# Kernel optimization log

Hardware: AMD Instinct MI355X
Metric: run time of the kernel (lower is better)

Reference implementation:

```python
import jax, jax.numpy as jnp
import numpy as np

PH = PW = 5  # roi_size
EPS = 1e-5


def _conv1x1(x, w, b):
    # x: (B,Cin,H,W), w: (Cout,Cin)
    return jnp.einsum('bchw,oc->bohw', x, w) + b[None, :, None, None]


def _resize_ac(x, oh, ow):
    # F.interpolate bilinear, align_corners=True. x: (B,C,H,W)
    B, C, H, W = x.shape
    ys = jnp.linspace(0.0, H - 1.0, oh)
    xs = jnp.linspace(0.0, W - 1.0, ow)
    y0 = jnp.floor(ys).astype(jnp.int32); y1 = jnp.minimum(y0 + 1, H - 1)
    x0 = jnp.floor(xs).astype(jnp.int32); x1 = jnp.minimum(x0 + 1, W - 1)
    ly = (ys - y0)[:, None]; lx = (xs - x0)[None, :]
    v00 = x[:, :, y0[:, None], x0[None, :]]
    v01 = x[:, :, y0[:, None], x1[None, :]]
    v10 = x[:, :, y1[:, None], x0[None, :]]
    v11 = x[:, :, y1[:, None], x1[None, :]]
    return v00 * (1 - ly) * (1 - lx) + v01 * (1 - ly) * lx + v10 * ly * (1 - lx) + v11 * ly * lx


def _roi_align_one(feat, box):
    # torchvision RoIAlign, spatial_scale=1, sampling_ratio=1, aligned=False
    # feat: (C,H,W), box: (x1,y1,x2,y2)
    C, H, W = feat.shape
    bx1, by1, bx2, by2 = box[0], box[1], box[2], box[3]
    rw = jnp.maximum(bx2 - bx1, 1.0)
    rh = jnp.maximum(by2 - by1, 1.0)
    xs = bx1 + (jnp.arange(PW, dtype=feat.dtype) + 0.5) * (rw / PW)
    ys = by1 + (jnp.arange(PH, dtype=feat.dtype) + 0.5) * (rh / PH)
    yg = jnp.broadcast_to(ys[:, None], (PH, PW))
    xg = jnp.broadcast_to(xs[None, :], (PH, PW))
    valid = (yg >= -1.0) & (yg <= H) & (xg >= -1.0) & (xg <= W)
    y = jnp.clip(yg, 0.0, H - 1.0); x = jnp.clip(xg, 0.0, W - 1.0)
    y0 = jnp.floor(y).astype(jnp.int32); x0 = jnp.floor(x).astype(jnp.int32)
    y1i = jnp.minimum(y0 + 1, H - 1); x1i = jnp.minimum(x0 + 1, W - 1)
    ly = y - y0; lx = x - x0
    v = (feat[:, y0, x0] * (1 - ly) * (1 - lx) + feat[:, y0, x1i] * (1 - ly) * lx
         + feat[:, y1i, x0] * ly * (1 - lx) + feat[:, y1i, x1i] * ly * lx)
    return v * valid  # (C,PH,PW)


def _layernorm(x, w, b):
    mu = jnp.mean(x, -1, keepdims=True)
    var = jnp.var(x, -1, keepdims=True)
    return (x - mu) * jax.lax.rsqrt(var + EPS) * w + b


def setup_inputs() -> dict:
    key = jax.random.key(0)
    ks = jax.random.split(key, 16)
    B, G, NB, HF = 8, 8, 16, 28
    x4 = jax.random.normal(ks[0], (B, 1024, 14, 14), jnp.float32)
    x5 = jax.random.normal(ks[1], (B, 2048, 7, 7), jnp.float32)
    bx = jax.random.uniform(ks[2], (B, NB), minval=0.0, maxval=18.0)
    by = jax.random.uniform(ks[3], (B, NB), minval=0.0, maxval=18.0)
    bw = jax.random.uniform(ks[4], (B, NB), minval=3.0, maxval=10.0)
    bh = jax.random.uniform(ks[5], (B, NB), minval=3.0, maxval=10.0)
    boxes = jnp.stack([bx, by, jnp.minimum(bx + bw, 28.0), jnp.minimum(by + bh, 28.0)], -1)
    group = jax.random.randint(ks[6], (B, G, 2), 0, NB, jnp.int32)
    real_in_num = jnp.full((B,), G, jnp.int32)
    label_s = jax.random.randint(ks[7], (B, G), 0, 6, jnp.int64)
    label_s = jnp.where(jnp.arange(G)[None, :] % 3 == 0, -1, label_s)  # exercise both branches
    skeleton = jax.random.normal(ks[8], (B, G, HF, HF), jnp.float32)
    D = 1536 * PH * PW  # 38400
    return {
        'x4': x4, 'x5': x5, 'boxes': boxes, 'skeleton': skeleton,
        'group': group, 'real_in_num': real_in_num, 'label_s': label_s,
        'conv1_w': jax.random.normal(ks[9], (), jnp.float32) * 0.5,
        'conv1_b': jax.random.normal(ks[10], (), jnp.float32) * 0.1,
        'conv2_w': jax.random.normal(ks[11], (512, 1024), jnp.float32) * 0.03,
        'conv2_b': jnp.zeros((512,), jnp.float32),
        'conv3_w': jax.random.normal(ks[12], (1024, 2048), jnp.float32) * 0.02,
        'conv3_b': jnp.zeros((1024,), jnp.float32),
        'norm1_w': jnp.ones((D,), jnp.float32), 'norm1_b': jnp.zeros((D,), jnp.float32),
        'norm2_w': jnp.ones((512,), jnp.float32), 'norm2_b': jnp.zeros((512,), jnp.float32),
        'fc1_w': jax.random.normal(ks[13], (512, D), jnp.float32) * float(np.sqrt(2.0 / D)),
        'fc1_b': jnp.zeros((512,), jnp.float32),
        'fc2_w': jax.random.normal(ks[14], (6, 512), jnp.float32) * float(np.sqrt(2.0 / 512)),
        'fc2_b': jnp.zeros((6,), jnp.float32),
    }


def reference(x4, x5, boxes, skeleton, group, real_in_num, label_s,
              conv1_w, conv1_b, conv2_w, conv2_b, conv3_w, conv3_b,
              norm1_w, norm1_b, norm2_w, norm2_b, fc1_w, fc1_b, fc2_w, fc2_b):
    B, G = skeleton.shape[0], skeleton.shape[1]
    HF, WF = skeleton.shape[2], skeleton.shape[3]
    # backbone heads: 1x1 conv + bilinear upsample (align_corners=True), concat
    f4 = _resize_ac(_conv1x1(x4, conv2_w, conv2_b), HF, WF)   # (B,512,28,28)
    f5 = _resize_ac(_conv1x1(x5, conv3_w, conv3_b), HF, WF)   # (B,1024,28,28)
    app = jnp.concatenate([f4, f5], axis=1)                   # (B,1536,28,28)
    C = app.shape[1]
    # per-person pose gate: 1x1 conv (scalar on single channel) + sigmoid
    gate = jax.nn.sigmoid(skeleton * conv1_w + conv1_b)       # (B,G,28,28)
    gated = gate[:, :, None] * app[:, None]                   # (B,G,C,28,28)
    use_gate = (label_s != -1)[:, :, None, None, None]
    pose_feature = jnp.where(use_gate, gated, app[:, None])   # (B,G,C,28,28)
    # union box of the two interacting people (get_box_tensor)
    bidx = jnp.arange(B)[:, None]
    b1 = boxes[bidx, group[..., 0]]                           # (B,G,4)
    b2 = boxes[bidx, group[..., 1]]
    ub = jnp.stack([jnp.minimum(b1[..., 0], b2[..., 0]), jnp.minimum(b1[..., 1], b2[..., 1]),
                    jnp.maximum(b1[..., 2], b2[..., 2]), jnp.maximum(b1[..., 3], b2[..., 3])], -1)
    # batched RoIAlign over all N = B*G boxes
    feats = pose_feature.reshape(B * G, C, HF, WF)
    rois = jax.vmap(_roi_align_one)(feats, ub.reshape(B * G, 4))  # (N,C,5,5)
    sk = rois.reshape(B * G, -1)                              # (N,38400)
    sk = jax.nn.relu(_layernorm(sk, norm1_w, norm1_b))
    # dropout(p=0.9) is identity in eval mode
    sk = sk @ fc1_w.T + fc1_b
    sk = _layernorm(sk, norm2_w, norm2_b)
    score = sk @ fc2_w.T + fc2_b                              # (N,6)
    return score
```

## Files before the change

kernel.cpp:

```cpp
#include <hip/hip_runtime.h>
#include <math.h>

#define B8   8
#define HW4  196
#define HW5  49
#define HFW  28
#define NPIX 784
#define CAPP 1536
#define D1   38400
#define NR   64

typedef short short8 __attribute__((ext_vector_type(8)));
typedef short short4v __attribute__((ext_vector_type(4)));
typedef float floatx16 __attribute__((ext_vector_type(16)));

__device__ __forceinline__ unsigned short f2bf(float f) {
  unsigned u = __float_as_uint(f);
  u += 0x7FFF + ((u >> 16) & 1);
  return (unsigned short)(u >> 16);
}

struct Params {
  const float *x4, *x5, *boxes, *skel;
  const int *group, *label;
  const float *c1w, *c1b, *w2c, *b2c, *w3c, *b3c;
  const float *n1w, *n1b, *n2w, *n2b, *fw1, *fb1, *fw2, *fb2;
  float* out;
  unsigned short *x4T, *x5T, *sknT;
  float *f4T, *f5T, *tap4w, *tap5w, *descw, *roisP, *stats, *out1;
  int *tap4o, *tap5o, *desco;
};

union SharedU {
  float tile[32 * 201];
  struct {
    unsigned short As[2][4096];
    unsigned short Bs[2][4096];
  } g;
  struct {
    float cw4[16], cw5[16], wgs;
    int co4[16], co5[16];
    float red[8];
  } roi;
  struct {
    float red[8];
    float red2[24];
  } ln;
};

__device__ __forceinline__ void gemm_unit(
    SharedU& sh, const unsigned short* __restrict__ A, const float* __restrict__ Bw,
    float* __restrict__ C, int mt, int nt, int k0, int kchunk,
    int K, int N, int Mvalid) {
  int t = threadIdx.x;
  int wave = t >> 6, lane = t & 63;
  int wm = wave & 1, wn = wave >> 1;
  const unsigned short* Aptr = A + (size_t)(mt * 64) * K + k0;
  const float* Bptr = Bw + (size_t)(nt * 64) * K + k0;
  short8 areg[2];
  float4 breg[4];
  floatx16 acc;
#pragma unroll
  for (int i = 0; i < 16; i++) acc[i] = 0.f;
  int nkb = kchunk >> 6;

#pragma unroll
  for (int i = 0; i < 2; i++) {
    int e = t + i * 256;
    areg[i] = *(const short8*)(Aptr + (size_t)(e >> 3) * K + (e & 7) * 8);
  }
#pragma unroll
  for (int i = 0; i < 4; i++) {
    int e = t + i * 256;
    breg[i] = *(const float4*)(Bptr + (size_t)(e >> 4) * K + (e & 15) * 4);
  }
#pragma unroll
  for (int i = 0; i < 2; i++) {
    int e = t + i * 256;
    int m = e >> 3, ko = e & 7;
    *(short8*)&sh.g.As[0][ko * 512 + ((m ^ ko)) * 8] = areg[i];
  }
#pragma unroll
  for (int i = 0; i < 4; i++) {
    int e = t + i * 256;
    short4v v;
    v[0] = (short)f2bf(breg[i].x); v[1] = (short)f2bf(breg[i].y);
    v[2] = (short)f2bf(breg[i].z); v[3] = (short)f2bf(breg[i].w);
    int ko = (e & 15) >> 1, half = (e & 15) & 1, n = e >> 4;
    *(short4v*)&sh.g.Bs[0][ko * 512 + ((n ^ ko)) * 8 + half * 4] = v;
  }
  __syncthreads();

  for (int kb = 0; kb < nkb; kb++) {
    int buf = kb & 1;
    bool more = (kb + 1) < nkb;
    if (more) {
      int kof = (kb + 1) * 64;
#pragma unroll
      for (int i = 0; i < 2; i++) {
        int e = t + i * 256;
        areg[i] = *(const short8*)(Aptr + (size_t)(e >> 3) * K + kof + (e & 7) * 8);
      }
#pragma unroll
      for (int i = 0; i < 4; i++) {
        int e = t + i * 256;
        breg[i] = *(const float4*)(Bptr + (size_t)(e >> 4) * K + kof + (e & 15) * 4);
      }
    }
#pragma unroll
    for (int s = 0; s < 4; s++) {
      int ko = 2 * s + (lane >> 5);
      int am = wm * 32 + (lane & 31);
      int bn = wn * 32 + (lane & 31);
      short8 af = *(const short8*)&sh.g.As[buf][ko * 512 + ((am ^ ko)) * 8];
      short8 bf = *(const short8*)&sh.g.Bs[buf][ko * 512 + ((bn ^ ko)) * 8];
      acc = __builtin_amdgcn_mfma_f32_32x32x16_bf16(af, bf, acc, 0, 0, 0);
    }
    __syncthreads();
    if (more) {
      int nb2 = 1 - buf;
#pragma unroll
      for (int i = 0; i < 2; i++) {
        int e = t + i * 256;
        int m = e >> 3, ko = e & 7;
        *(short8*)&sh.g.As[nb2][ko * 512 + ((m ^ ko)) * 8] = areg[i];
      }
#pragma unroll
      for (int i = 0; i < 4; i++) {
        int e = t + i * 256;
        short4v v;
        v[0] = (short)f2bf(breg[i].x); v[1] = (short)f2bf(breg[i].y);
        v[2] = (short)f2bf(breg[i].z); v[3] = (short)f2bf(breg[i].w);
        int ko = (e & 15) >> 1, half = (e & 15) & 1, n = e >> 4;
        *(short4v*)&sh.g.Bs[nb2][ko * 512 + ((n ^ ko)) * 8 + half * 4] = v;
      }
      __syncthreads();
    }
  }

  int col = nt * 64 + wn * 32 + (lane & 31);
  int rbase = mt * 64 + wm * 32 + 4 * (lane >> 5);
#pragma unroll
  for (int reg = 0; reg < 16; reg++) {
    int row = rbase + (reg & 3) + 8 * (reg >> 2);
    if (row < Mvalid) atomicAdd(&C[(size_t)row * N + col], acc[reg]);
  }
}

__device__ __forceinline__ float gate_val(const float* sk, int yy, int xx,
                                          float c1w, float c1b, bool use) {
  if (!use) return 1.f;
  float z = sk[yy * HFW + xx] * c1w + c1b;
  return 1.f / (1.f + expf(-z));
}

__device__ void run_phase(const Params& p, int phase, SharedU& sh) {
  int bid = blockIdx.x, t = threadIdx.x, gb = gridDim.x;
  int gtid = bid * 256 + t;
  int nth = gb * 256;

  if (phase == 0) {
    float4 z4 = make_float4(0.f, 0.f, 0.f, 0.f);
    for (int i = gtid; i < 319488; i += nth) ((float4*)p.f4T)[i] = z4;
    for (int i = gtid; i < 8192; i += nth) ((float4*)p.out1)[i] = z4;
    if (gtid < 128) p.stats[gtid] = 0.f;

    for (int u = bid; u < 836; u += gb) {
      __syncthreads();
      if (u < 256) {
        int b = u >> 5, cc = u & 31;
        for (int i = t; i < 32 * HW4; i += 256) {
          int c = i / HW4, hw = i - c * HW4;
          sh.tile[c * 201 + hw] = p.x4[((size_t)(b * 1024 + cc * 32 + c)) * HW4 + hw];
        }
        __syncthreads();
        for (int i = t; i < HW4 * 32; i += 256) {
          int hw = i >> 5, c = i & 31;
          p.x4T[((size_t)(b * HW4 + hw)) * 1024 + cc * 32 + c] = f2bf(sh.tile[c * 201 + hw]);
        }
      } else if (u < 768) {
        int u2 = u - 256;
        int b = u2 >> 6, cc = u2 & 63;
        for (int i = t; i < 32 * HW5; i += 256) {
          int c = i / HW5, hw = i - c * HW5;
          sh.tile[c * 51 + hw] = p.x5[((size_t)(b * 2048 + cc * 32 + c)) * HW5 + hw];
        }
        __syncthreads();
        for (int i = t; i < HW5 * 32; i += 256) {
          int hw = i >> 5, c = i & 31;
          p.x5T[((size_t)(b * HW5 + hw)) * 2048 + cc * 32 + c] = f2bf(sh.tile[c * 51 + hw]);
        }
      } else if (u < 832) {
        int bg = u - 768;
        if (t < 25) {
          int b = bg >> 3;
          int i1 = p.group[bg * 2 + 0], i2 = p.group[bg * 2 + 1];
          const float* bb1 = p.boxes + (size_t)(b * 16 + i1) * 4;
          const float* bb2 = p.boxes + (size_t)(b * 16 + i2) * 4;
          float ux1 = fminf(bb1[0], bb2[0]);
          float uy1 = fminf(bb1[1], bb2[1]);
          float ux2 = fmaxf(bb1[2], bb2[2]);
          float uy2 = fmaxf(bb1[3], bb2[3]);
          float rw = fmaxf(ux2 - ux1, 1.0f), rh = fmaxf(uy2 - uy1, 1.0f);
          int iy = t / 5, ix = t % 5;
          float sy = uy1 + (iy + 0.5f) * (rh * 0.2f);
          float sx = ux1 + (ix + 0.5f) * (rw * 0.2f);
          float valid = (sy >= -1.0f && sy <= 28.0f && sx >= -1.0f && sx <= 28.0f) ? 1.f : 0.f;
          float y = fminf(fmaxf(sy, 0.f), 27.f);
          float x = fminf(fmaxf(sx, 0.f), 27.f);
          int y0 = (int)floorf(y), x0 = (int)floorf(x);
          int y1 = min(y0 + 1, 27), x1 = min(x0 + 1, 27);
          float ly = y - (float)y0, lx = x - (float)x0;
          bool use = (p.label[bg] != -1);
          float c1w = p.c1w[0], c1b = p.c1b[0];
          const float* sk = p.skel + (size_t)bg * NPIX;
          int idx = (bg * 25 + t) * 4;
          p.descw[idx + 0] = (1.f - ly) * (1.f - lx) * valid * gate_val(sk, y0, x0, c1w, c1b, use);
          p.descw[idx + 1] = (1.f - ly) * lx * valid * gate_val(sk, y0, x1, c1w, c1b, use);
          p.descw[idx + 2] = ly * (1.f - lx) * valid * gate_val(sk, y1, x0, c1w, c1b, use);
          p.descw[idx + 3] = ly * lx * valid * gate_val(sk, y1, x1, c1w, c1b, use);
          p.desco[idx + 0] = y0 * HFW + x0;
          p.desco[idx + 1] = y0 * HFW + x1;
          p.desco[idx + 2] = y1 * HFW + x0;
          p.desco[idx + 3] = y1 * HFW + x1;
        }
      } else {
        int pix = (u - 832) * 196 + t;
        if (t < 196) {
          int y = pix / HFW, x = pix % HFW;
          {
            float sy = y * (13.0f / 27.0f), sx = x * (13.0f / 27.0f);
            int y0 = (int)sy, x0 = (int)sx;
            int y1 = min(y0 + 1, 13), x1 = min(x0 + 1, 13);
            float ly = sy - y0, lx = sx - x0;
            p.tap4o[pix * 4 + 0] = y0 * 14 + x0; p.tap4w[pix * 4 + 0] = (1.f - ly) * (1.f - lx);
            p.tap4o[pix * 4 + 1] = y0 * 14 + x1; p.tap4w[pix * 4 + 1] = (1.f - ly) * lx;
            p.tap4o[pix * 4 + 2] = y1 * 14 + x0; p.tap4w[pix * 4 + 2] = ly * (1.f - lx);
            p.tap4o[pix * 4 + 3] = y1 * 14 + x1; p.tap4w[pix * 4 + 3] = ly * lx;
          }
          {
            float sy = y * (6.0f / 27.0f), sx = x * (6.0f / 27.0f);
            int y0 = (int)sy, x0 = (int)sx;
            int y1 = min(y0 + 1, 6), x1 = min(x0 + 1, 6);
            float ly = sy - y0, lx = sx - x0;
            p.tap5o[pix * 4 + 0] = y0 * 7 + x0; p.tap5w[pix * 4 + 0] = (1.f - ly) * (1.f - lx);
            p.tap5o[pix * 4 + 1] = y0 * 7 + x1; p.tap5w[pix * 4 + 1] = (1.f - ly) * lx;
            p.tap5o[pix * 4 + 2] = y1 * 7 + x0; p.tap5w[pix * 4 + 2] = ly * (1.f - lx);
            p.tap5o[pix * 4 + 3] = y1 * 7 + x1; p.tap5w[pix * 4 + 3] = ly * lx;
          }
        }
      }
    }

  } else if (phase == 1) {
    for (int u = bid; u < 1696; u += gb) {
      __syncthreads();
      if (u < 800) {
        int mt = u % 25, r = u / 25;
        int nt = r & 7, sp = r >> 3;
        gemm_unit(sh, p.x4T, p.w2c, p.f4T, mt, nt, sp * 256, 256, 1024, 512, 1568);
      } else {
        int u2 = u - 800;
        int mt = u2 % 7, r = u2 / 7;
        int nt = r & 15, sp = r >> 4;
        gemm_unit(sh, p.x5T, p.w3c, p.f5T, mt, nt, sp * 256, 256, 2048, 1024, 392);
      }
    }

  } else if (phase == 2) {
    for (int u = bid; u < 1600; u += gb) {
      __syncthreads();
      int pp = u % 25, bg = u / 25, b = bg >> 3;
      int di = (bg * 25 + pp) * 4;
      if (t < 16) {
        int i = t >> 2, j = t & 3;
        float wg = p.descw[di + i];
        int pix = p.desco[di + i];
        sh.roi.cw4[t] = wg * p.tap4w[pix * 4 + j];
        sh.roi.co4[t] = (b * HW4 + p.tap4o[pix * 4 + j]) * 512;
        sh.roi.cw5[t] = wg * p.tap5w[pix * 4 + j];
        sh.roi.co5[t] = (b * HW5 + p.tap5o[pix * 4 + j]) * 1024;
      }
      if (t == 16) sh.roi.wgs = p.descw[di] + p.descw[di + 1] + p.descw[di + 2] + p.descw[di + 3];
      __syncthreads();
      float w4r[16], w5r[16];
      int o4r[16], o5r[16];
      float wg = sh.roi.wgs;
#pragma unroll
      for (int i = 0; i < 16; i++) {
        w4r[i] = sh.roi.cw4[i]; o4r[i] = sh.roi.co4[i];
        w5r[i] = sh.roi.cw5[i]; o5r[i] = sh.roi.co5[i];
      }
      float ls = 0.f, ls2 = 0.f;
      float* outp = p.roisP + (size_t)(bg * 25 + pp) * CAPP;
      for (int c = t; c < 512; c += 256) {
        float acc = wg * p.b2c[c];
#pragma unroll
        for (int i = 0; i < 16; i++) acc = fmaf(w4r[i], p.f4T[o4r[i] + c], acc);
        outp[c] = acc;
        ls += acc; ls2 = fmaf(acc, acc, ls2);
      }
      for (int c = t; c < 1024; c += 256) {
        float acc = wg * p.b3c[c];
#pragma unroll
        for (int i = 0; i < 16; i++) acc = fmaf(w5r[i], p.f5T[o5r[i] + c], acc);
        outp[512 + c] = acc;
        ls += acc; ls2 = fmaf(acc, acc, ls2);
      }
      for (int off = 32; off; off >>= 1) {
        ls += __shfl_down(ls, off);
        ls2 += __shfl_down(ls2, off);
      }
      int wv = t >> 6;
      if ((t & 63) == 0) { sh.roi.red[wv] = ls; sh.roi.red[4 + wv] = ls2; }
      __syncthreads();
      if (t == 0) {
        atomicAdd(&p.stats[bg * 2 + 0], sh.roi.red[0] + sh.roi.red[1] + sh.roi.red[2] + sh.roi.red[3]);
        atomicAdd(&p.stats[bg * 2 + 1], sh.roi.red[4] + sh.roi.red[5] + sh.roi.red[6] + sh.roi.red[7]);
      }
    }

  } else if (phase == 3) {
    for (int u = bid; u < 384; u += gb) {
      __syncthreads();
      int r = u / 6, ch = u - r * 6;
      int c0 = ch * 256;
      float S = p.stats[r * 2], S2 = p.stats[r * 2 + 1];
      float mu = S * (1.f / D1);
      float var = S2 * (1.f / D1) - mu * mu;
      float rs = rsqrtf(var + 1e-5f);
      const float* rp = p.roisP + (size_t)r * 25 * CAPP + c0;
#pragma unroll
      for (int pp = 0; pp < 25; pp++)
        sh.tile[pp * 257 + t] = rp[(size_t)pp * CAPP + t];
      __syncthreads();
      unsigned short* op = p.sknT + (size_t)r * D1 + c0 * 25;
      const float* wv = p.n1w + c0 * 25;
      const float* bv = p.n1b + c0 * 25;
      for (int j = t; j < 6400; j += 256) {
        unsigned cc = (unsigned)j / 25u;
        unsigned pp = (unsigned)j - cc * 25u;
        float x = sh.tile[pp * 257 + cc];
        float v = fmaf((x - mu) * rs, wv[j], bv[j]);
        op[j] = f2bf(fmaxf(v, 0.f));
      }
    }

  } else if (phase == 4) {
    for (int u = bid; u < 960; u += gb) {
      __syncthreads();
      int nt = u & 7, sp = u >> 3;
      gemm_unit(sh, p.sknT, p.fw1, p.out1, 0, nt, sp * 320, 320, 38400, 512, 64);
    }

  } else {
    for (int r = bid; r < NR; r += gb) {
      __syncthreads();
      int j1 = t, j2 = t + 256;
      float v1 = p.out1[r * 512 + j1] + p.fb1[j1];
      float v2 = p.out1[r * 512 + j2] + p.fb1[j2];
      float s = v1 + v2, s2 = v1 * v1 + v2 * v2;
      for (int off = 32; off; off >>= 1) {
        s += __shfl_down(s, off);
        s2 += __shfl_down(s2, off);
      }
      int wv = t >> 6;
      if ((t & 63) == 0) { sh.ln.red[wv] = s; sh.ln.red[4 + wv] = s2; }
      __syncthreads();
      float S = sh.ln.red[0] + sh.ln.red[1] + sh.ln.red[2] + sh.ln.red[3];
      float S2 = sh.ln.red[4] + sh.ln.red[5] + sh.ln.red[6] + sh.ln.red[7];
      float mu = S / 512.f;
      float var = S2 / 512.f - mu * mu;
      float rs = rsqrtf(var + 1e-5f);
      float n1v = fmaf((v1 - mu) * rs, p.n2w[j1], p.n2b[j1]);
      float n2v = fmaf((v2 - mu) * rs, p.n2w[j2], p.n2b[j2]);
      float pm[6];
#pragma unroll
      for (int m = 0; m < 6; m++)
        pm[m] = n1v * p.fw2[m * 512 + j1] + n2v * p.fw2[m * 512 + j2];
#pragma unroll
      for (int m = 0; m < 6; m++)
        for (int off = 32; off; off >>= 1) pm[m] += __shfl_down(pm[m], off);
      if ((t & 63) == 0) {
#pragma unroll
        for (int m = 0; m < 6; m++) sh.ln.red2[wv * 6 + m] = pm[m];
      }
      __syncthreads();
      if (t < 6)
        p.out[r * 6 + t] = sh.ln.red2[t] + sh.ln.red2[6 + t] + sh.ln.red2[12 + t] +
                           sh.ln.red2[18 + t] + p.fb2[t];
    }
  }
}

__global__ __launch_bounds__(256, 4) void phase_kernel(Params p, int phase) {
  __shared__ SharedU sh;
  run_phase(p, phase, sh);
}

extern "C" void kernel_launch(void* const* d_in, const int* in_sizes, int n_in,
                              void* d_out, int out_size, void* d_ws, size_t ws_size,
                              hipStream_t stream) {
  Params p;
  p.x4    = (const float*)d_in[0];
  p.x5    = (const float*)d_in[1];
  p.boxes = (const float*)d_in[2];
  p.skel  = (const float*)d_in[3];
  p.group = (const int*)d_in[4];
  p.label = (const int*)d_in[6];
  p.c1w   = (const float*)d_in[7];
  p.c1b   = (const float*)d_in[8];
  p.w2c   = (const float*)d_in[9];
  p.b2c   = (const float*)d_in[10];
  p.w3c   = (const float*)d_in[11];
  p.b3c   = (const float*)d_in[12];
  p.n1w   = (const float*)d_in[13];
  p.n1b   = (const float*)d_in[14];
  p.n2w   = (const float*)d_in[15];
  p.n2b   = (const float*)d_in[16];
  p.fw1   = (const float*)d_in[17];
  p.fb1   = (const float*)d_in[18];
  p.fw2   = (const float*)d_in[19];
  p.fb2   = (const float*)d_in[20];
  p.out   = (float*)d_out;

  float* ws = (float*)d_ws;
  p.x4T   = (unsigned short*)ws;
  p.x5T   = (unsigned short*)(ws + 819200);
  p.f4T   = ws + 1277952;
  p.f5T   = ws + 2097152;
  p.tap4w = ws + 2555904;
  p.tap4o = (int*)(ws + 2559040);
  p.tap5w = ws + 2562176;
  p.tap5o = (int*)(ws + 2565312);
  p.descw = ws + 2568448;
  p.desco = (int*)(ws + 2574848);
  p.roisP = ws + 2581248;
  p.stats = ws + 5038848;
  p.sknT  = (unsigned short*)(ws + 5038976);
  p.out1  = ws + 6267776;

  phase_kernel<<<836,  256, 0, stream>>>(p, 0);
  phase_kernel<<<1696, 256, 0, stream>>>(p, 1);
  phase_kernel<<<1600, 256, 0, stream>>>(p, 2);
  phase_kernel<<<384,  256, 0, stream>>>(p, 3);
  phase_kernel<<<960,  256, 0, stream>>>(p, 4);
  phase_kernel<<<64,   256, 0, stream>>>(p, 5);
}
```

Before: 246.8 us.

## Replace split-K atomics with full-K stores and partial-sum buffers for GEMMs

The x4 conv GEMM now runs over the full K with plain stores instead of four split-K slices combined by atomics, so its output no longer needs zeroing. The x5 GEMM uses larger K chunks with fewer atomics. The fc1 GEMM writes per-split partial tiles into a 60-slice buffer that the final phase sums, replacing the atomics and the zeroing of the accumulator. This removes atomic traffic and memset work, but gives fewer blocks in phase 1 and more partial-sum reads in phase 5.

```diff
diff --git a/kernel.cpp b/kernel.cpp
--- a/kernel.cpp
+++ b/kernel.cpp
@@ -27,7 +27,7 @@
   const float *n1w, *n1b, *n2w, *n2b, *fw1, *fb1, *fw2, *fb2;
   float* out;
   unsigned short *x4T, *x5T, *sknT;
-  float *f4T, *f5T, *tap4w, *tap5w, *descw, *roisP, *stats, *out1;
+  float *f4T, *f5T, *tap4w, *tap5w, *descw, *roisP, *stats, *fc1P;
   int *tap4o, *tap5o, *desco;
 };
 
@@ -51,7 +51,7 @@
 __device__ __forceinline__ void gemm_unit(
     SharedU& sh, const unsigned short* __restrict__ A, const float* __restrict__ Bw,
     float* __restrict__ C, int mt, int nt, int k0, int kchunk,
-    int K, int N, int Mvalid) {
+    int K, int N, int Mvalid, bool accum) {
   int t = threadIdx.x;
   int wave = t >> 6, lane = t & 63;
   int wm = wave & 1, wn = wave >> 1;
@@ -140,10 +140,18 @@
 
   int col = nt * 64 + wn * 32 + (lane & 31);
   int rbase = mt * 64 + wm * 32 + 4 * (lane >> 5);
-#pragma unroll
-  for (int reg = 0; reg < 16; reg++) {
-    int row = rbase + (reg & 3) + 8 * (reg >> 2);
-    if (row < Mvalid) atomicAdd(&C[(size_t)row * N + col], acc[reg]);
+  if (accum) {
+#pragma unroll
+    for (int reg = 0; reg < 16; reg++) {
+      int row = rbase + (reg & 3) + 8 * (reg >> 2);
+      if (row < Mvalid) atomicAdd(&C[(size_t)row * N + col], acc[reg]);
+    }
+  } else {
+#pragma unroll
+    for (int reg = 0; reg < 16; reg++) {
+      int row = rbase + (reg & 3) + 8 * (reg >> 2);
+      if (row < Mvalid) C[(size_t)row * N + col] = acc[reg];
+    }
   }
 }
 
@@ -161,8 +169,7 @@
 
   if (phase == 0) {
     float4 z4 = make_float4(0.f, 0.f, 0.f, 0.f);
-    for (int i = gtid; i < 319488; i += nth) ((float4*)p.f4T)[i] = z4;
-    for (int i = gtid; i < 8192; i += nth) ((float4*)p.out1)[i] = z4;
+    for (int i = gtid; i < 114688; i += nth) ((float4*)p.f5T)[i] = z4;
     if (gtid < 128) p.stats[gtid] = 0.f;
 
     for (int u = bid; u < 836; u += gb) {
@@ -253,17 +260,16 @@
     }
 
   } else if (phase == 1) {
-    for (int u = bid; u < 1696; u += gb) {
-      __syncthreads();
-      if (u < 800) {
-        int mt = u % 25, r = u / 25;
-        int nt = r & 7, sp = r >> 3;
-        gemm_unit(sh, p.x4T, p.w2c, p.f4T, mt, nt, sp * 256, 256, 1024, 512, 1568);
+    for (int u = bid; u < 424; u += gb) {
+      __syncthreads();
+      if (u < 200) {
+        int mt = u % 25, nt = u / 25;
+        gemm_unit(sh, p.x4T, p.w2c, p.f4T, mt, nt, 0, 1024, 1024, 512, 1568, false);
       } else {
-        int u2 = u - 800;
+        int u2 = u - 200;
         int mt = u2 % 7, r = u2 / 7;
         int nt = r & 15, sp = r >> 4;
-        gemm_unit(sh, p.x5T, p.w3c, p.f5T, mt, nt, sp * 256, 256, 2048, 1024, 392);
+        gemm_unit(sh, p.x5T, p.w3c, p.f5T, mt, nt, sp * 1024, 1024, 2048, 1024, 392, true);
       }
     }
 
@@ -347,18 +353,24 @@
     }
 
   } else if (phase == 4) {
-    for (int u = bid; u < 960; u += gb) {
+    for (int u = bid; u < 480; u += gb) {
       __syncthreads();
       int nt = u & 7, sp = u >> 3;
-      gemm_unit(sh, p.sknT, p.fw1, p.out1, 0, nt, sp * 320, 320, 38400, 512, 64);
+      gemm_unit(sh, p.sknT, p.fw1, p.fc1P + (size_t)sp * (NR * 512),
+                0, nt, sp * 640, 640, 38400, 512, 64, false);
     }
 
   } else {
     for (int r = bid; r < NR; r += gb) {
       __syncthreads();
       int j1 = t, j2 = t + 256;
-      float v1 = p.out1[r * 512 + j1] + p.fb1[j1];
-      float v2 = p.out1[r * 512 + j2] + p.fb1[j2];
+      float v1 = p.fb1[j1], v2 = p.fb1[j2];
+      const float* pq = p.fc1P + (size_t)r * 512;
+#pragma unroll 10
+      for (int s = 0; s < 60; s++) {
+        v1 += pq[(size_t)s * (NR * 512) + j1];
+        v2 += pq[(size_t)s * (NR * 512) + j2];
+      }
       float s = v1 + v2, s2 = v1 * v1 + v2 * v2;
       for (int off = 32; off; off >>= 1) {
         s += __shfl_down(s, off);
@@ -438,12 +450,12 @@
   p.roisP = ws + 2581248;
   p.stats = ws + 5038848;
   p.sknT  = (unsigned short*)(ws + 5038976);
-  p.out1  = ws + 6267776;
+  p.fc1P  = ws + 6267776;
 
   phase_kernel<<<836,  256, 0, stream>>>(p, 0);
-  phase_kernel<<<1696, 256, 0, stream>>>(p, 1);
+  phase_kernel<<<424,  256, 0, stream>>>(p, 1);
   phase_kernel<<<1600, 256, 0, stream>>>(p, 2);
   phase_kernel<<<384,  256, 0, stream>>>(p, 3);
-  phase_kernel<<<960,  256, 0, stream>>>(p, 4);
+  phase_kernel<<<480,  256, 0, stream>>>(p, 4);
   phase_kernel<<<64,   256, 0, stream>>>(p, 5);
 }
```

Measured after the change: 269.2 us. 9.1% more time.

## Replace fc1 split-K atomics with partial buffers and separate reduction kernel

Applied to the files above, without the earlier changes.

The fc1 GEMM now writes per-split partial results to a dedicated buffer with plain stores instead of atomically adding into out1, using 100 K-splits of 384 instead of 120 of 320. A new kernel reduces the partials and adds the bias, and the LayerNorm/fc2 kernel reads the reduced result. The single phase-switch kernel is also split into separate specialised kernels, which may reduce register pressure per phase. This removes atomic contention and the out1 zeroing, at the cost of an extra launch and roughly 13 MB of partial-buffer traffic.

```diff
diff --git a/kernel.cpp b/kernel.cpp
--- a/kernel.cpp
+++ b/kernel.cpp
@@ -9,6 +9,7 @@
 #define CAPP 1536
 #define D1   38400
 #define NR   64
+#define NSP  100
 
 typedef short short8 __attribute__((ext_vector_type(8)));
 typedef short short4v __attribute__((ext_vector_type(4)));
@@ -27,7 +28,7 @@
   const float *n1w, *n1b, *n2w, *n2b, *fw1, *fb1, *fw2, *fb2;
   float* out;
   unsigned short *x4T, *x5T, *sknT;
-  float *f4T, *f5T, *tap4w, *tap5w, *descw, *roisP, *stats, *out1;
+  float *f4T, *f5T, *tap4w, *tap5w, *descw, *roisP, *stats, *fc1P, *out1;
   int *tap4o, *tap5o, *desco;
 };
 
@@ -51,7 +52,7 @@
 __device__ __forceinline__ void gemm_unit(
     SharedU& sh, const unsigned short* __restrict__ A, const float* __restrict__ Bw,
     float* __restrict__ C, int mt, int nt, int k0, int kchunk,
-    int K, int N, int Mvalid) {
+    int K, int N, int Mvalid, bool accum) {
   int t = threadIdx.x;
   int wave = t >> 6, lane = t & 63;
   int wm = wave & 1, wn = wave >> 1;
@@ -140,10 +141,18 @@
 
   int col = nt * 64 + wn * 32 + (lane & 31);
   int rbase = mt * 64 + wm * 32 + 4 * (lane >> 5);
-#pragma unroll
-  for (int reg = 0; reg < 16; reg++) {
-    int row = rbase + (reg & 3) + 8 * (reg >> 2);
-    if (row < Mvalid) atomicAdd(&C[(size_t)row * N + col], acc[reg]);
+  if (accum) {
+#pragma unroll
+    for (int reg = 0; reg < 16; reg++) {
+      int row = rbase + (reg & 3) + 8 * (reg >> 2);
+      if (row < Mvalid) atomicAdd(&C[(size_t)row * N + col], acc[reg]);
+    }
+  } else {
+#pragma unroll
+    for (int reg = 0; reg < 16; reg++) {
+      int row = rbase + (reg & 3) + 8 * (reg >> 2);
+      if (row < Mvalid) C[(size_t)row * N + col] = acc[reg];
+    }
   }
 }
 
@@ -154,249 +163,276 @@
   return 1.f / (1.f + expf(-z));
 }
 
-__device__ void run_phase(const Params& p, int phase, SharedU& sh) {
+__device__ void run_phase0(const Params& p, SharedU& sh) {
   int bid = blockIdx.x, t = threadIdx.x, gb = gridDim.x;
   int gtid = bid * 256 + t;
   int nth = gb * 256;
-
-  if (phase == 0) {
-    float4 z4 = make_float4(0.f, 0.f, 0.f, 0.f);
-    for (int i = gtid; i < 319488; i += nth) ((float4*)p.f4T)[i] = z4;
-    for (int i = gtid; i < 8192; i += nth) ((float4*)p.out1)[i] = z4;
-    if (gtid < 128) p.stats[gtid] = 0.f;
-
-    for (int u = bid; u < 836; u += gb) {
+  float4 z4 = make_float4(0.f, 0.f, 0.f, 0.f);
+  for (int i = gtid; i < 319488; i += nth) ((float4*)p.f4T)[i] = z4;
+  if (gtid < 128) p.stats[gtid] = 0.f;
+
+  for (int u = bid; u < 836; u += gb) {
+    __syncthreads();
+    if (u < 256) {
+      int b = u >> 5, cc = u & 31;
+      for (int i = t; i < 32 * HW4; i += 256) {
+        int c = i / HW4, hw = i - c * HW4;
+        sh.tile[c * 201 + hw] = p.x4[((size_t)(b * 1024 + cc * 32 + c)) * HW4 + hw];
+      }
       __syncthreads();
-      if (u < 256) {
-        int b = u >> 5, cc = u & 31;
-        for (int i = t; i < 32 * HW4; i += 256) {
-          int c = i / HW4, hw = i - c * HW4;
-          sh.tile[c * 201 + hw] = p.x4[((size_t)(b * 1024 + cc * 32 + c)) * HW4 + hw];
+      for (int i = t; i < HW4 * 32; i += 256) {
+        int hw = i >> 5, c = i & 31;
+        p.x4T[((size_t)(b * HW4 + hw)) * 1024 + cc * 32 + c] = f2bf(sh.tile[c * 201 + hw]);
+      }
+    } else if (u < 768) {
+      int u2 = u - 256;
+      int b = u2 >> 6, cc = u2 & 63;
+      for (int i = t; i < 32 * HW5; i += 256) {
+        int c = i / HW5, hw = i - c * HW5;
+        sh.tile[c * 51 + hw] = p.x5[((size_t)(b * 2048 + cc * 32 + c)) * HW5 + hw];
+      }
+      __syncthreads();
+      for (int i = t; i < HW5 * 32; i += 256) {
+        int hw = i >> 5, c = i & 31;
+        p.x5T[((size_t)(b * HW5 + hw)) * 2048 + cc * 32 + c] = f2bf(sh.tile[c * 51 + hw]);
+      }
+    } else if (u < 832) {
+      int bg = u - 768;
+      if (t < 25) {
+        int b = bg >> 3;
+        int i1 = p.group[bg * 2 + 0], i2 = p.group[bg * 2 + 1];
+        const float* bb1 = p.boxes + (size_t)(b * 16 + i1) * 4;
+        const float* bb2 = p.boxes + (size_t)(b * 16 + i2) * 4;
+        float ux1 = fminf(bb1[0], bb2[0]);
+        float uy1 = fminf(bb1[1], bb2[1]);
+        float ux2 = fmaxf(bb1[2], bb2[2]);
+        float uy2 = fmaxf(bb1[3], bb2[3]);
+        float rw = fmaxf(ux2 - ux1, 1.0f), rh = fmaxf(uy2 - uy1, 1.0f);
+        int iy = t / 5, ix = t % 5;
+        float sy = uy1 + (iy + 0.5f) * (rh * 0.2f);
+        float sx = ux1 + (ix + 0.5f) * (rw * 0.2f);
+        float valid = (sy >= -1.0f && sy <= 28.0f && sx >= -1.0f && sx <= 28.0f) ? 1.f : 0.f;
+        float y = fminf(fmaxf(sy, 0.f), 27.f);
+        float x = fminf(fmaxf(sx, 0.f), 27.f);
+        int y0 = (int)floorf(y), x0 = (int)floorf(x);
+        int y1 = min(y0 + 1, 27), x1 = min(x0 + 1, 27);
+        float ly = y - (float)y0, lx = x - (float)x0;
+        bool use = (p.label[bg] != -1);
+        float c1w = p.c1w[0], c1b = p.c1b[0];
+        const float* sk = p.skel + (size_t)bg * NPIX;
+        int idx = (bg * 25 + t) * 4;
+        p.descw[idx + 0] = (1.f - ly) * (1.f - lx) * valid * gate_val(sk, y0, x0, c1w, c1b, use);
+        p.descw[idx + 1] = (1.f - ly) * lx * valid * gate_val(sk, y0, x1, c1w, c1b, use);
+        p.descw[idx + 2] = ly * (1.f - lx) * valid * gate_val(sk, y1, x0, c1w, c1b, use);
+        p.descw[idx + 3] = ly * lx * valid * gate_val(sk, y1, x1, c1w, c1b, use);
+        p.desco[idx + 0] = y0 * HFW + x0;
+        p.desco[idx + 1] = y0 * HFW + x1;
+        p.desco[idx + 2] = y1 * HFW + x0;
+        p.desco[idx + 3] = y1 * HFW + x1;
+      }
+    } else {
+      int pix = (u - 832) * 196 + t;
+      if (t < 196) {
+        int y = pix / HFW, x = pix % HFW;
+        {
+          float sy = y * (13.0f / 27.0f), sx = x * (13.0f / 27.0f);
+          int y0 = (int)sy, x0 = (int)sx;
+          int y1 = min(y0 + 1, 13), x1 = min(x0 + 1, 13);
+          float ly = sy - y0, lx = sx - x0;
+          p.tap4o[pix * 4 + 0] = y0 * 14 + x0; p.tap4w[pix * 4 + 0] = (1.f - ly) * (1.f - lx);
+          p.tap4o[pix * 4 + 1] = y0 * 14 + x1; p.tap4w[pix * 4 + 1] = (1.f - ly) * lx;
+          p.tap4o[pix * 4 + 2] = y1 * 14 + x0; p.tap4w[pix * 4 + 2] = ly * (1.f - lx);
+          p.tap4o[pix * 4 + 3] = y1 * 14 + x1; p.tap4w[pix * 4 + 3] = ly * lx;
         }
-        __syncthreads();
-        for (int i = t; i < HW4 * 32; i += 256) {
-          int hw = i >> 5, c = i & 31;
-          p.x4T[((size_t)(b * HW4 + hw)) * 1024 + cc * 32 + c] = f2bf(sh.tile[c * 201 + hw]);
+        {
+          float sy = y * (6.0f / 27.0f), sx = x * (6.0f / 27.0f);
+          int y0 = (int)sy, x0 = (int)sx;
+          int y1 = min(y0 + 1, 6), x1 = min(x0 + 1, 6);
+          float ly = sy - y0, lx = sx - x0;
+          p.tap5o[pix * 4 + 0] = y0 * 7 + x0; p.tap5w[pix * 4 + 0] = (1.f - ly) * (1.f - lx);
+          p.tap5o[pix * 4 + 1] = y0 * 7 + x1; p.tap5w[pix * 4 + 1] = (1.f - ly) * lx;
+          p.tap5o[pix * 4 + 2] = y1 * 7 + x0; p.tap5w[pix * 4 + 2] = ly * (1.f - lx);
+          p.tap5o[pix * 4 + 3] = y1 * 7 + x1; p.tap5w[pix * 4 + 3] = ly * lx;
         }
-      } else if (u < 768) {
-        int u2 = u - 256;
-        int b = u2 >> 6, cc = u2 & 63;
-        for (int i = t; i < 32 * HW5; i += 256) {
-          int c = i / HW5, hw = i - c * HW5;
-          sh.tile[c * 51 + hw] = p.x5[((size_t)(b * 2048 + cc * 32 + c)) * HW5 + hw];
-        }
-        __syncthreads();
-        for (int i = t; i < HW5 * 32; i += 256) {
-          int hw = i >> 5, c = i & 31;
-          p.x5T[((size_t)(b * HW5 + hw)) * 2048 + cc * 32 + c] = f2bf(sh.tile[c * 51 + hw]);
-        }
-      } else if (u < 832) {
-        int bg = u - 768;
-        if (t < 25) {
-          int b = bg >> 3;
-          int i1 = p.group[bg * 2 + 0], i2 = p.group[bg * 2 + 1];
-          const float* bb1 = p.boxes + (size_t)(b * 16 + i1) * 4;
-          const float* bb2 = p.boxes + (size_t)(b * 16 + i2) * 4;
-          float ux1 = fminf(bb1[0], bb2[0]);
-          float uy1 = fminf(bb1[1], bb2[1]);
-          float ux2 = fmaxf(bb1[2], bb2[2]);
-          float uy2 = fmaxf(bb1[3], bb2[3]);
-          float rw = fmaxf(ux2 - ux1, 1.0f), rh = fmaxf(uy2 - uy1, 1.0f);
-          int iy = t / 5, ix = t % 5;
-          float sy = uy1 + (iy + 0.5f) * (rh * 0.2f);
-          float sx = ux1 + (ix + 0.5f) * (rw * 0.2f);
-          float valid = (sy >= -1.0f && sy <= 28.0f && sx >= -1.0f && sx <= 28.0f) ? 1.f : 0.f;
-          float y = fminf(fmaxf(sy, 0.f), 27.f);
-          float x = fminf(fmaxf(sx, 0.f), 27.f);
-          int y0 = (int)floorf(y), x0 = (int)floorf(x);
-          int y1 = min(y0 + 1, 27), x1 = min(x0 + 1, 27);
-          float ly = y - (float)y0, lx = x - (float)x0;
-          bool use = (p.label[bg] != -1);
-          float c1w = p.c1w[0], c1b = p.c1b[0];
-          const float* sk = p.skel + (size_t)bg * NPIX;
-          int idx = (bg * 25 + t) * 4;
-          p.descw[idx + 0] = (1.f - ly) * (1.f - lx) * valid * gate_val(sk, y0, x0, c1w, c1b, use);
-          p.descw[idx + 1] = (1.f - ly) * lx * valid * gate_val(sk, y0, x1, c1w, c1b, use);
-          p.descw[idx + 2] = ly * (1.f - lx) * valid * gate_val(sk, y1, x0, c1w, c1b, use);
-          p.descw[idx + 3] = ly * lx * valid * gate_val(sk, y1, x1, c1w, c1b, use);
-          p.desco[idx + 0] = y0 * HFW + x0;
-          p.desco[idx + 1] = y0 * HFW + x1;
-          p.desco[idx + 2] = y1 * HFW + x0;
-          p.desco[idx + 3] = y1 * HFW + x1;
-        }
-      } else {
-        int pix = (u - 832) * 196 + t;
-        if (t < 196) {
-          int y = pix / HFW, x = pix % HFW;
-          {
-            float sy = y * (13.0f / 27.0f), sx = x * (13.0f / 27.0f);
-            int y0 = (int)sy, x0 = (int)sx;
-            int y1 = min(y0 + 1, 13), x1 = min(x0 + 1, 13);
-            float ly = sy - y0, lx = sx - x0;
-            p.tap4o[pix * 4 + 0] = y0 * 14 + x0; p.tap4w[pix * 4 + 0] = (1.f - ly) * (1.f - lx);
-            p.tap4o[pix * 4 + 1] = y0 * 14 + x1; p.tap4w[pix * 4 + 1] = (1.f - ly) * lx;
-            p.tap4o[pix * 4 + 2] = y1 * 14 + x0; p.tap4w[pix * 4 + 2] = ly * (1.f - lx);
-            p.tap4o[pix * 4 + 3] = y1 * 14 + x1; p.tap4w[pix * 4 + 3] = ly * lx;
-          }
-          {
-            float sy = y * (6.0f / 27.0f), sx = x * (6.0f / 27.0f);
-            int y0 = (int)sy, x0 = (int)sx;
-            int y1 = min(y0 + 1, 6), x1 = min(x0 + 1, 6);
-            float ly = sy - y0, lx = sx - x0;
-            p.tap5o[pix * 4 + 0] = y0 * 7 + x0; p.tap5w[pix * 4 + 0] = (1.f - ly) * (1.f - lx);
-            p.tap5o[pix * 4 + 1] = y0 * 7 + x1; p.tap5w[pix * 4 + 1] = (1.f - ly) * lx;
-            p.tap5o[pix * 4 + 2] = y1 * 7 + x0; p.tap5w[pix * 4 + 2] = ly * (1.f - lx);
-            p.tap5o[pix * 4 + 3] = y1 * 7 + x1; p.tap5w[pix * 4 + 3] = ly * lx;
-          }
-        }
-      }
-    }
-
-  } else if (phase == 1) {
-    for (int u = bid; u < 1696; u += gb) {
-      __syncthreads();
-      if (u < 800) {
-        int mt = u % 25, r = u / 25;
-        int nt = r & 7, sp = r >> 3;
-        gemm_unit(sh, p.x4T, p.w2c, p.f4T, mt, nt, sp * 256, 256, 1024, 512, 1568);
-      } else {
-        int u2 = u - 800;
-        int mt = u2 % 7, r = u2 / 7;
-        int nt = r & 15, sp = r >> 4;
-        gemm_unit(sh, p.x5T, p.w3c, p.f5T, mt, nt, sp * 256, 256, 2048, 1024, 392);
-      }
-    }
-
-  } else if (phase == 2) {
-    for (int u = bid; u < 1600; u += gb) {
-      __syncthreads();
-      int pp = u % 25, bg = u / 25, b = bg >> 3;
-      int di = (bg * 25 + pp) * 4;
-      if (t < 16) {
-        int i = t >> 2, j = t & 3;
-        float wg = p.descw[di + i];
-        int pix = p.desco[di + i];
-        sh.roi.cw4[t] = wg * p.tap4w[pix * 4 + j];
-        sh.roi.co4[t] = (b * HW4 + p.tap4o[pix * 4 + j]) * 512;
-        sh.roi.cw5[t] = wg * p.tap5w[pix * 4 + j];
-        sh.roi.co5[t] = (b * HW5 + p.tap5o[pix * 4 + j]) * 1024;
-      }
-      if (t == 16) sh.roi.wgs = p.descw[di] + p.descw[di + 1] + p.descw[di + 2] + p.descw[di + 3];
-      __syncthreads();
-      float w4r[16], w5r[16];
-      int o4r[16], o5r[16];
-      float wg = sh.roi.wgs;
-#pragma unroll
-      for (int i = 0; i < 16; i++) {
-        w4r[i] = sh.roi.cw4[i]; o4r[i] = sh.roi.co4[i];
-        w5r[i] = sh.roi.cw5[i]; o5r[i] = sh.roi.co5[i];
-      }
-      float ls = 0.f, ls2 = 0.f;
-      float* outp = p.roisP + (size_t)(bg * 25 + pp) * CAPP;
-      for (int c = t; c < 512; c += 256) {
-        float acc = wg * p.b2c[c];
-#pragma unroll
-        for (int i = 0; i < 16; i++) acc = fmaf(w4r[i], p.f4T[o4r[i] + c], acc);
-        outp[c] = acc;
-        ls += acc; ls2 = fmaf(acc, acc, ls2);
-      }
-      for (int c = t; c < 1024; c += 256) {
-        float acc = wg * p.b3c[c];
-#pragma unroll
-        for (int i = 0; i < 16; i++) acc = fmaf(w5r[i], p.f5T[o5r[i] + c], acc);
-        outp[512 + c] = acc;
-        ls += acc; ls2 = fmaf(acc, acc, ls2);
-      }
-      for (int off = 32; off; off >>= 1) {
-        ls += __shfl_down(ls, off);
-        ls2 += __shfl_down(ls2, off);
-      }
-      int wv = t >> 6;
-      if ((t & 63) == 0) { sh.roi.red[wv] = ls; sh.roi.red[4 + wv] = ls2; }
-      __syncthreads();
-      if (t == 0) {
-        atomicAdd(&p.stats[bg * 2 + 0], sh.roi.red[0] + sh.roi.red[1] + sh.roi.red[2] + sh.roi.red[3]);
-        atomicAdd(&p.stats[bg * 2 + 1], sh.roi.red[4] + sh.roi.red[5] + sh.roi.red[6] + sh.roi.red[7]);
-      }
-    }
-
-  } else if (phase == 3) {
-    for (int u = bid; u < 384; u += gb) {
-      __syncthreads();
-      int r = u / 6, ch = u - r * 6;
-      int c0 = ch * 256;
-      float S = p.stats[r * 2], S2 = p.stats[r * 2 + 1];
-      float mu = S * (1.f / D1);
-      float var = S2 * (1.f / D1) - mu * mu;
-      float rs = rsqrtf(var + 1e-5f);
-      const float* rp = p.roisP + (size_t)r * 25 * CAPP + c0;
-#pragma unroll
-      for (int pp = 0; pp < 25; pp++)
-        sh.tile[pp * 257 + t] = rp[(size_t)pp * CAPP + t];
-      __syncthreads();
-      unsigned short* op = p.sknT + (size_t)r * D1 + c0 * 25;
-      const float* wv = p.n1w + c0 * 25;
-      const float* bv = p.n1b + c0 * 25;
-      for (int j = t; j < 6400; j += 256) {
-        unsigned cc = (unsigned)j / 25u;
-        unsigned pp = (unsigned)j - cc * 25u;
-        float x = sh.tile[pp * 257 + cc];
-        float v = fmaf((x - mu) * rs, wv[j], bv[j]);
-        op[j] = f2bf(fmaxf(v, 0.f));
-      }
-    }
-
-  } else if (phase == 4) {
-    for (int u = bid; u < 960; u += gb) {
-      __syncthreads();
-      int nt = u & 7, sp = u >> 3;
-      gemm_unit(sh, p.sknT, p.fw1, p.out1, 0, nt, sp * 320, 320, 38400, 512, 64);
-    }
-
-  } else {
-    for (int r = bid; r < NR; r += gb) {
-      __syncthreads();
-      int j1 = t, j2 = t + 256;
-      float v1 = p.out1[r * 512 + j1] + p.fb1[j1];
-      float v2 = p.out1[r * 512 + j2] + p.fb1[j2];
-      float s = v1 + v2, s2 = v1 * v1 + v2 * v2;
-      for (int off = 32; off; off >>= 1) {
-        s += __shfl_down(s, off);
-        s2 += __shfl_down(s2, off);
-      }
-      int wv = t >> 6;
-      if ((t & 63) == 0) { sh.ln.red[wv] = s; sh.ln.red[4 + wv] = s2; }
-      __syncthreads();
-      float S = sh.ln.red[0] + sh.ln.red[1] + sh.ln.red[2] + sh.ln.red[3];
-      float S2 = sh.ln.red[4] + sh.ln.red[5] + sh.ln.red[6] + sh.ln.red[7];
-      float mu = S / 512.f;
-      float var = S2 / 512.f - mu * mu;
-      float rs = rsqrtf(var + 1e-5f);
-      float n1v = fmaf((v1 - mu) * rs, p.n2w[j1], p.n2b[j1]);
-      float n2v = fmaf((v2 - mu) * rs, p.n2w[j2], p.n2b[j2]);
-      float pm[6];
-#pragma unroll
-      for (int m = 0; m < 6; m++)
-        pm[m] = n1v * p.fw2[m * 512 + j1] + n2v * p.fw2[m * 512 + j2];
-#pragma unroll
-      for (int m = 0; m < 6; m++)
-        for (int off = 32; off; off >>= 1) pm[m] += __shfl_down(pm[m], off);
-      if ((t & 63) == 0) {
-#pragma unroll
-        for (int m = 0; m < 6; m++) sh.ln.red2[wv * 6 + m] = pm[m];
-      }
-      __syncthreads();
-      if (t < 6)
-        p.out[r * 6 + t] = sh.ln.red2[t] + sh.ln.red2[6 + t] + sh.ln.red2[12 + t] +
-                           sh.ln.red2[18 + t] + p.fb2[t];
-    }
-  }
-}
-
-__global__ __launch_bounds__(256, 4) void phase_kernel(Params p, int phase) {
-  __shared__ SharedU sh;
-  run_phase(p, phase, sh);
-}
+      }
+    }
+  }
+}
+
+__device__ void run_phase1(const Params& p, SharedU& sh) {
+  int bid = blockIdx.x, gb = gridDim.x;
+  for (int u = bid; u < 1696; u += gb) {
+    __syncthreads();
+    if (u < 800) {
+      int mt = u % 25, r = u / 25;
+      int nt = r & 7, sp = r >> 3;
+      gemm_unit(sh, p.x4T, p.w2c, p.f4T, mt, nt, sp * 256, 256, 1024, 512, 1568, true);
+    } else {
+      int u2 = u - 800;
+      int mt = u2 % 7, r = u2 / 7;
+      int nt = r & 15, sp = r >> 4;
+      gemm_unit(sh, p.x5T, p.w3c, p.f5T, mt, nt, sp * 256, 256, 2048, 1024, 392, true);
+    }
+  }
+}
+
+__device__ void run_phase2(const Params& p, SharedU& sh) {
+  int bid = blockIdx.x, t = threadIdx.x, gb = gridDim.x;
+  for (int u = bid; u < 1600; u += gb) {
+    __syncthreads();
+    int pp = u % 25, bg = u / 25, b = bg >> 3;
+    int di = (bg * 25 + pp) * 4;
+    if (t < 16) {
+      int i = t >> 2, j = t & 3;
+      float wg = p.descw[di + i];
+      int pix = p.desco[di + i];
+      sh.roi.cw4[t] = wg * p.tap4w[pix * 4 + j];
+      sh.roi.co4[t] = (b * HW4 + p.tap4o[pix * 4 + j]) * 512;
+      sh.roi.cw5[t] = wg * p.tap5w[pix * 4 + j];
+      sh.roi.co5[t] = (b * HW5 + p.tap5o[pix * 4 + j]) * 1024;
+    }
+    if (t == 16) sh.roi.wgs = p.descw[di] + p.descw[di + 1] + p.descw[di + 2] + p.descw[di + 3];
+    __syncthreads();
+    float w4r[16], w5r[16];
+    int o4r[16], o5r[16];
+    float wg = sh.roi.wgs;
+#pragma unroll
+    for (int i = 0; i < 16; i++) {
+      w4r[i] = sh.roi.cw4[i]; o4r[i] = sh.roi.co4[i];
+      w5r[i] = sh.roi.cw5[i]; o5r[i] = sh.roi.co5[i];
+    }
+    float ls = 0.f, ls2 = 0.f;
+    float* outp = p.roisP + (size_t)(bg * 25 + pp) * CAPP;
+    for (int c = t; c < 512; c += 256) {
+      float acc = wg * p.b2c[c];
+#pragma unroll
+      for (int i = 0; i < 16; i++) acc = fmaf(w4r[i], p.f4T[o4r[i] + c], acc);
+      outp[c] = acc;
+      ls += acc; ls2 = fmaf(acc, acc, ls2);
+    }
+    for (int c = t; c < 1024; c += 256) {
+      float acc = wg * p.b3c[c];
+#pragma unroll
+      for (int i = 0; i < 16; i++) acc = fmaf(w5r[i], p.f5T[o5r[i] + c], acc);
+      outp[512 + c] = acc;
+      ls += acc; ls2 = fmaf(acc, acc, ls2);
+    }
+    for (int off = 32; off; off >>= 1) {
+      ls += __shfl_down(ls, off);
+      ls2 += __shfl_down(ls2, off);
+    }
+    int wv = t >> 6;
+    if ((t & 63) == 0) { sh.roi.red[wv] = ls; sh.roi.red[4 + wv] = ls2; }
+    __syncthreads();
+    if (t == 0) {
+      atomicAdd(&p.stats[bg * 2 + 0], sh.roi.red[0] + sh.roi.red[1] + sh.roi.red[2] + sh.roi.red[3]);
+      atomicAdd(&p.stats[bg * 2 + 1], sh.roi.red[4] + sh.roi.red[5] + sh.roi.red[6] + sh.roi.red[7]);
+    }
+  }
+}
+
+__device__ void run_phase3(const Params& p, SharedU& sh) {
+  int bid = blockIdx.x, t = threadIdx.x, gb = gridDim.x;
+  for (int u = bid; u < 384; u += gb) {
+    __syncthreads();
+    int r = u / 6, ch = u - r * 6;
+    int c0 = ch * 256;
+    float S = p.stats[r * 2], S2 = p.stats[r * 2 + 1];
+    float mu = S * (1.f / D1);
+    float var = S2 * (1.f / D1) - mu * mu;
+    float rs = rsqrtf(var + 1e-5f);
+    const float* rp = p.roisP + (size_t)r * 25 * CAPP + c0;
+#pragma unroll
+    for (int pp = 0; pp < 25; pp++)
+      sh.tile[pp * 257 + t] = rp[(size_t)pp * CAPP + t];
+    __syncthreads();
+    unsigned short* op = p.sknT + (size_t)r * D1 + c0 * 25;
+    const float* wv = p.n1w + c0 * 25;
+    const float* bv = p.n1b + c0 * 25;
+    for (int j = t; j < 6400; j += 256) {
+      unsigned cc = (unsigned)j / 25u;
+      unsigned pp = (unsigned)j - cc * 25u;
+      float x = sh.tile[pp * 257 + cc];
+      float v = fmaf((x - mu) * rs, wv[j], bv[j]);
+      op[j] = f2bf(fmaxf(v, 0.f));
+    }
+  }
+}
+
+__device__ void run_phase4(const Params& p, SharedU& sh) {
+  int bid = blockIdx.x, gb = gridDim.x;
+  for (int u = bid; u < 8 * NSP; u += gb) {
+    __syncthreads();
+    int nt = u & 7, sp = u >> 3;
+    gemm_unit(sh, p.sknT, p.fw1, p.fc1P + (size_t)sp * (NR * 512),
+              0, nt, sp * 384, 384, 38400, 512, 64, false);
+  }
+}
+
+__device__ void run_phase5a(const Params& p, SharedU& sh) {
+  int bid = blockIdx.x, t = threadIdx.x;
+  int r = bid >> 3, cb = bid & 7;
+  int c = cb * 64 + (t & 63), sg = t >> 6;
+  const float* pq = p.fc1P + (size_t)r * 512 + c;
+  float v = 0.f;
+#pragma unroll 5
+  for (int s = sg * 25; s < sg * 25 + 25; s++)
+    v += pq[(size_t)s * (NR * 512)];
+  sh.tile[sg * 64 + (t & 63)] = v;
+  __syncthreads();
+  if (t < 64) {
+    float r0 = sh.tile[t] + sh.tile[64 + t] + sh.tile[128 + t] + sh.tile[192 + t];
+    p.out1[(size_t)r * 512 + cb * 64 + t] = r0 + p.fb1[cb * 64 + t];
+  }
+}
+
+__device__ void run_phase5b(const Params& p, SharedU& sh) {
+  int bid = blockIdx.x, t = threadIdx.x, gb = gridDim.x;
+  for (int r = bid; r < NR; r += gb) {
+    __syncthreads();
+    int j1 = t, j2 = t + 256;
+    float v1 = p.out1[r * 512 + j1];
+    float v2 = p.out1[r * 512 + j2];
+    float s = v1 + v2, s2 = v1 * v1 + v2 * v2;
+    for (int off = 32; off; off >>= 1) {
+      s += __shfl_down(s, off);
+      s2 += __shfl_down(s2, off);
+    }
+    int wv = t >> 6;
+    if ((t & 63) == 0) { sh.ln.red[wv] = s; sh.ln.red[4 + wv] = s2; }
+    __syncthreads();
+    float S = sh.ln.red[0] + sh.ln.red[1] + sh.ln.red[2] + sh.ln.red[3];
+    float S2 = sh.ln.red[4] + sh.ln.red[5] + sh.ln.red[6] + sh.ln.red[7];
+    float mu = S / 512.f;
+    float var = S2 / 512.f - mu * mu;
+    float rs = rsqrtf(var + 1e-5f);
+    float n1v = fmaf((v1 - mu) * rs, p.n2w[j1], p.n2b[j1]);
+    float n2v = fmaf((v2 - mu) * rs, p.n2w[j2], p.n2b[j2]);
+    float pm[6];
+#pragma unroll
+    for (int m = 0; m < 6; m++)
+      pm[m] = n1v * p.fw2[m * 512 + j1] + n2v * p.fw2[m * 512 + j2];
+#pragma unroll
+    for (int m = 0; m < 6; m++)
+      for (int off = 32; off; off >>= 1) pm[m] += __shfl_down(pm[m], off);
+    if ((t & 63) == 0) {
+#pragma unroll
+      for (int m = 0; m < 6; m++) sh.ln.red2[wv * 6 + m] = pm[m];
+    }
+    __syncthreads();
+    if (t < 6)
+      p.out[r * 6 + t] = sh.ln.red2[t] + sh.ln.red2[6 + t] + sh.ln.red2[12 + t] +
+                         sh.ln.red2[18 + t] + p.fb2[t];
+  }
+}
+
+__global__ __launch_bounds__(256, 4) void k_phase0(Params p) { __shared__ SharedU sh; run_phase0(p, sh); }
+__global__ __launch_bounds__(256, 4) void k_phase1(Params p) { __shared__ SharedU sh; run_phase1(p, sh); }
+__global__ __launch_bounds__(256, 4) void k_phase2(Params p) { __shared__ SharedU sh; run_phase2(p, sh); }
+__global__ __launch_bounds__(256, 4) void k_phase3(Params p) { __shared__ SharedU sh; run_phase3(p, sh); }
+__global__ __launch_bounds__(256, 4) void k_phase4(Params p) { __shared__ SharedU sh; run_phase4(p, sh); }
+__global__ __launch_bounds__(256, 4) void k_phase5a(Params p) { __shared__ SharedU sh; run_phase5a(p, sh); }
+__global__ __launch_bounds__(256, 4) void k_phase5b(Params p) { __shared__ SharedU sh; run_phase5b(p, sh); }
 
 extern "C" void kernel_launch(void* const* d_in, const int* in_sizes, int n_in,
                               void* d_out, int out_size, void* d_ws, size_t ws_size,
@@ -438,12 +474,14 @@
   p.roisP = ws + 2581248;
   p.stats = ws + 5038848;
   p.sknT  = (unsigned short*)(ws + 5038976);
-  p.out1  = ws + 6267776;
-
-  phase_kernel<<<836,  256, 0, stream>>>(p, 0);
-  phase_kernel<<<1696, 256, 0, stream>>>(p, 1);
-  phase_kernel<<<1600, 256, 0, stream>>>(p, 2);
-  phase_kernel<<<384,  256, 0, stream>>>(p, 3);
-  phase_kernel<<<960,  256, 0, stream>>>(p, 4);
-  phase_kernel<<<64,   256, 0, stream>>>(p, 5);
-}
+  p.fc1P  = ws + 6267776;
+  p.out1  = ws + 9544576;
+
+  k_phase0<<<836,  256, 0, stream>>>(p);
+  k_phase1<<<1696, 256, 0, stream>>>(p);
+  k_phase2<<<1600, 256, 0, stream>>>(p);
+  k_phase3<<<384,  256, 0, stream>>>(p);
+  k_phase4<<<800,  256, 0, stream>>>(p);
+  k_phase5a<<<512, 256, 0, stream>>>(p);
+  k_phase5b<<<64,  256, 0, stream>>>(p);
+}
```

Measured after the change: 256.0 us. 3.8% more time.
